# Optimization experiments

Measured on AMD Instinct MI355X. Metric: run time of the kernel, lower is better.

## Reference

```python
import jax, jax.numpy as jnp
import numpy as np

N = 50000
E = 800000
D = 128          # in_channels == hidden_channels
L = 3            # num_layers
JK = D * L       # jk 'cat' output
H2 = D // 2      # classifier hidden
C = 2            # out classes
EPS = 1e-5


def setup_inputs() -> dict:
    key = jax.random.key(0)
    ks = jax.random.split(key, 16)
    x = jax.random.normal(ks[0], (N, D), dtype=jnp.float32)
    edge_index = jax.random.randint(ks[1], (2, E), 0, N, dtype=jnp.int64)
    s = 0.05
    Wl = jax.random.normal(ks[2], (L, D, D), dtype=jnp.float32) * s   # lin_l (on aggregated), has bias
    bl = jax.random.normal(ks[3], (L, D), dtype=jnp.float32) * s
    Wr = jax.random.normal(ks[4], (L, D, D), dtype=jnp.float32) * s   # lin_r (on root), no bias
    gamma = jnp.ones((L, D), dtype=jnp.float32)
    beta = jnp.zeros((L, D), dtype=jnp.float32)
    rmean = jax.random.normal(ks[5], (L, D), dtype=jnp.float32) * s
    rvar = jax.random.uniform(ks[6], (L, D), dtype=jnp.float32, minval=0.5, maxval=1.5)
    Wc1 = jax.random.normal(ks[7], (JK, H2), dtype=jnp.float32) * s
    bc1 = jax.random.normal(ks[8], (H2,), dtype=jnp.float32) * s
    Wc2 = jax.random.normal(ks[9], (H2, C), dtype=jnp.float32) * s
    bc2 = jax.random.normal(ks[10], (C,), dtype=jnp.float32) * s
    return {"x": x, "edge_index": edge_index, "Wl": Wl, "bl": bl, "Wr": Wr,
            "gamma": gamma, "beta": beta, "rmean": rmean, "rvar": rvar,
            "Wc1": Wc1, "bc1": bc1, "Wc2": Wc2, "bc2": bc2}


def reference(x, edge_index, Wl, bl, Wr, gamma, beta, rmean, rvar, Wc1, bc1, Wc2, bc2):
    src, dst = edge_index[0], edge_index[1]
    # node in-degree (for mean aggregation), clamp to avoid div-by-zero
    deg = jax.ops.segment_sum(jnp.ones((E,), dtype=x.dtype), dst, num_segments=N)
    inv_deg = 1.0 / jnp.maximum(deg, 1.0)  # [N]

    h = x
    layer_outputs = []
    for i in range(L):
        # SAGEConv(mean): out = lin_l(mean_{j in N(i)} h_j) + lin_r(h_i)
        agg = jax.ops.segment_sum(h[src], dst, num_segments=N) * inv_deg[:, None]  # [N, D]
        h = agg @ Wl[i] + bl[i] + h @ Wr[i]
        # BatchNorm (eval: running stats), then ReLU; Dropout is identity in eval
        h = (h - rmean[i]) * jax.lax.rsqrt(rvar[i] + EPS) * gamma[i] + beta[i]
        h = jax.nn.relu(h)
        layer_outputs.append(h)

    jk = jnp.concatenate(layer_outputs, axis=-1)  # [N, L*D]
    z = jax.nn.relu(jk @ Wc1 + bc1)
    logits = z @ Wc2 + bc2  # [N, 2]
    return logits
```

## Files before the change

### kernel.cpp

```cpp
#include <hip/hip_runtime.h>
#include <hip/hip_fp16.h>
#include <cstdint>
#include <cstddef>

#define DD 128
#define JKD 384
#define EPSV 1e-5f
#define BSH 7
#define NBMAX 512
#define BCAP2 4096
#define PCH 8192
#define PTH 1024
#define BCAP 8192

typedef __attribute__((ext_vector_type(8))) short bf16x8;
typedef __attribute__((ext_vector_type(4))) float f32x4;
#define MFMA(a, b, c) __builtin_amdgcn_mfma_f32_16x16x32_bf16(a, b, c, 0, 0, 0)

__device__ inline unsigned short f2bf_rne(float f) {
  unsigned u = __float_as_uint(f);
  unsigned r = u + 0x7fffu + ((u >> 16) & 1u);
  return (unsigned short)(r >> 16);
}

__device__ inline void split8(const float* s, bf16x8& hi, bf16x8& lo) {
#pragma unroll
  for (int j = 0; j < 8; ++j) {
    float f = s[j];
    unsigned short h = f2bf_rne(f);
    float fh = __uint_as_float((unsigned)h << 16);
    hi[j] = (short)h;
    lo[j] = (short)f2bf_rne(f - fh);
  }
}

__device__ inline void h8_to_f8(uint4 raw, float* out) {
  const __half2* hp = reinterpret_cast<const __half2*>(&raw);
#pragma unroll
  for (int j = 0; j < 4; ++j) {
    float2 f = __half22float2(hp[j]);
    out[2 * j] = f.x;
    out[2 * j + 1] = f.y;
  }
}

__global__ void init_cursor(int* __restrict__ cursor) {
  int t = threadIdx.x;
  if (t < NBMAX) cursor[t] = t * BCAP2;
}

__global__ __launch_bounds__(PTH) void partition_prep(
    const int* __restrict__ src, const int* __restrict__ dst, int* bucket_cursor,
    unsigned* __restrict__ packed, int E, int nChunks,
    const float* __restrict__ Wl, const float* __restrict__ Wr, bf16x8* __restrict__ wf,
    const float* __restrict__ Wc1, bf16x8* __restrict__ wcf,
    const float* __restrict__ x, unsigned short* __restrict__ x16, int N) {
  __shared__ int h[NBMAX];
  __shared__ int lofs[NBMAX];
  __shared__ int res[NBMAX];
  __shared__ int lcur[NBMAX];
  __shared__ int wsum[4];
  __shared__ int wpref[4];
  __shared__ unsigned stage[PCH];

  if (blockIdx.x < nChunks) {
    int t = threadIdx.x;
    int lane = t & 63;
    int base = blockIdx.x * PCH;
    for (int i = t; i < NBMAX; i += PTH) h[i] = 0;
    __syncthreads();
#pragma unroll
    for (int it = 0; it < PCH / PTH; ++it) {
      int e = base + it * PTH + t;
      if (e < E) {
        int d = __builtin_nontemporal_load(dst + e);
        atomicAdd(&h[d >> BSH], 1);
      }
    }
    __syncthreads();
    int c0 = 0, c1 = 0, s = 0, sc = 0;
    if (t < 256) {
      c0 = h[2 * t];
      c1 = h[2 * t + 1];
      s = c0 + c1;
      sc = s;
#pragma unroll
      for (int off = 1; off < 64; off <<= 1) {
        int u = __shfl_up(sc, off, 64);
        if (lane >= off) sc += u;
      }
      if (lane == 63) wsum[t >> 6] = sc;
    }
    __syncthreads();
    if (t == 0) {
      int a = 0;
#pragma unroll
      for (int w = 0; w < 4; ++w) { wpref[w] = a; a += wsum[w]; }
    }
    __syncthreads();
    if (t < 256) {
      int excl = wpref[t >> 6] + sc - s;
      lofs[2 * t] = excl;
      lofs[2 * t + 1] = excl + c0;
      lcur[2 * t] = excl;
      lcur[2 * t + 1] = excl + c0;
      if (c0 > 0) res[2 * t] = atomicAdd(&bucket_cursor[2 * t], c0);
      if (c1 > 0) res[2 * t + 1] = atomicAdd(&bucket_cursor[2 * t + 1], c1);
    }
    __syncthreads();
#pragma unroll
    for (int it = 0; it < PCH / PTH; ++it) {
      int e = base + it * PTH + t;
      if (e < E) {
        int d = __builtin_nontemporal_load(dst + e);
        int sv = __builtin_nontemporal_load(src + e);
        int pos = atomicAdd(&lcur[d >> BSH], 1);
        stage[pos] = ((unsigned)(d & ((1 << BSH) - 1)) << 16) | (unsigned)(sv & 0xffff);
      }
    }
    __syncthreads();
    int wid = t >> 6;
    for (int b = wid; b < NBMAX; b += PTH / 64) {
      int run = h[b];
      if (run == 0) continue;
      int gbase = res[b], lbase = lofs[b];
      for (int j = lane; j < run; j += 64) packed[gbase + j] = stage[lbase + j];
    }
  } else {
    int sub = threadIdx.x >> 8;
    int t = threadIdx.x & 255;
    int f16blocks = (N * 16 + 255) / 256;
    int vb = (blockIdx.x - nChunks) * 4 + sub;
    if (vb >= 60 + f16blocks) return;
    if (vb < 48) {
      int idx = vb * 256 + t;
      int ln = idx & 63;
      int ksnt = (idx >> 6) & 31;
      int mat = (idx >> 11) & 1;
      int layer = idx >> 12;
      int ks = ksnt >> 3, nt = ksnt & 7;
      int nn = nt * 16 + (ln & 15);
      int k0 = ks * 32 + (ln >> 4) * 8;
      const float* W = (mat ? Wr : Wl) + (size_t)layer * DD * DD;
      float v[8];
#pragma unroll
      for (int j = 0; j < 8; ++j) v[j] = W[(size_t)(k0 + j) * DD + nn];
      bf16x8 hi, lo;
      split8(v, hi, lo);
      size_t base = (size_t)((layer * 2 + mat) * 2) * 2048 + (size_t)ksnt * 64 + ln;
      wf[base] = hi;
      wf[base + 2048] = lo;
    } else if (vb < 60) {
      int idx = (vb - 48) * 256 + t;
      int ln = idx & 63;
      int ksnt = idx >> 6;
      int ks = ksnt >> 2, nt = ksnt & 3;
      int nn = nt * 16 + (ln & 15);
      int k0 = ks * 32 + (ln >> 4) * 8;
      float v[8];
#pragma unroll
      for (int j = 0; j < 8; ++j) v[j] = Wc1[(size_t)(k0 + j) * 64 + nn];
      bf16x8 hi, lo;
      split8(v, hi, lo);
      wcf[idx] = hi;
      wcf[idx + 3072] = lo;
    } else {
      int idx = (vb - 60) * 256 + t;
      int r = idx >> 4, cc = (idx & 15) * 8;
      if (r < N) {
        const float* p = x + (size_t)r * DD + cc;
        float4 a = *reinterpret_cast<const float4*>(p);
        float4 bb = *reinterpret_cast<const float4*>(p + 4);
        __half2 h0 = __floats2half2_rn(a.x, a.y);
        __half2 h1 = __floats2half2_rn(a.z, a.w);
        __half2 h2 = __floats2half2_rn(bb.x, bb.y);
        __half2 h3 = __floats2half2_rn(bb.z, bb.w);
        uint4 o;
        o.x = *reinterpret_cast<unsigned*>(&h0);
        o.y = *reinterpret_cast<unsigned*>(&h1);
        o.z = *reinterpret_cast<unsigned*>(&h2);
        o.w = *reinterpret_cast<unsigned*>(&h3);
        *reinterpret_cast<uint4*>(x16 + (size_t)r * DD + cc) = o;
      }
    }
  }
}

__global__ __launch_bounds__(256) void csr_build(const unsigned* __restrict__ packed,
                                                 const int* __restrict__ bucket_cursor,
                                                 int* __restrict__ row_start,
                                                 int* __restrict__ row_end,
                                                 float* __restrict__ inv_deg,
                                                 unsigned short* __restrict__ col, int N) {
  __shared__ int cntA[128];
  __shared__ int lcur[128];
  __shared__ int wsum2[2];
  __shared__ int wpref2[2];
  __shared__ unsigned short stage[BCAP];
  int t = threadIdx.x;
  int b = blockIdx.x;
  int s0 = b * BCAP2;
  int cnt = bucket_cursor[b] - s0;
  if (t < 128) cntA[t] = 0;
  __syncthreads();
  for (int i = t; i < cnt; i += 256) {
    unsigned p = packed[s0 + i];
    atomicAdd(&cntA[p >> 16], 1);
  }
  __syncthreads();
  if (t < 128) {
    int lane = t & 63, wid = t >> 6;
    int v = cntA[t];
    int sc = v;
#pragma unroll
    for (int off = 1; off < 64; off <<= 1) {
      int u = __shfl_up(sc, off, 64);
      if (lane >= off) sc += u;
    }
    if (lane == 63) wsum2[wid] = sc;
    __syncthreads();
    if (t == 0) { wpref2[0] = 0; wpref2[1] = wsum2[0]; }
    __syncthreads();
    int excl = wpref2[wid] + sc - v;
    lcur[t] = excl;
    int node = b * 128 + t;
    if (node < N) {
      row_start[node] = s0 + excl;
      row_end[node] = s0 + excl + v;
      inv_deg[node] = 1.0f / fmaxf((float)v, 1.0f);
    }
  } else {
    __syncthreads();
    __syncthreads();
  }
  __syncthreads();
  for (int i = t; i < cnt; i += 256) {
    unsigned p = packed[s0 + i];
    int pos = atomicAdd(&lcur[p >> 16], 1);
    unsigned short us = (unsigned short)(p & 0xffff);
    if (pos < BCAP) stage[pos] = us;
    else col[s0 + pos] = us;
  }
  __syncthreads();
  int lim = min(cnt, BCAP);
  for (int i = t; i < lim; i += 256) col[s0 + i] = stage[i];
}

__global__ __launch_bounds__(256) void agg16_kernel(const unsigned short* __restrict__ h16,
                                                    int ldh,
                                                    const int* __restrict__ row_start,
                                                    const int* __restrict__ row_end,
                                                    const unsigned short* __restrict__ col,
                                                    const float* __restrict__ inv_deg,
                                                    unsigned short* __restrict__ agg16, int n) {
  int wib = threadIdx.x >> 6;
  int lane = threadIdx.x & 63;
  int node = blockIdx.x * 4 + wib;
  if (node >= n) return;
  int beg = row_start[node];
  int end = row_end[node];
  int q = lane >> 4, l15 = lane & 15;
  float acc[8];
#pragma unroll
  for (int k = 0; k < 8; ++k) acc[k] = 0.f;

  for (int j0 = beg; j0 < end; j0 += 16) {
    int cnt = end - j0;
    if (cnt > 16) cnt = 16;
    int cidx = (int)col[j0 + min(l15, cnt - 1)];
    uint4 raw[4];
    bool val[4];
#pragma unroll
    for (int k = 0; k < 4; ++k) {
      int e = k * 4 + q;
      int s = __shfl(cidx, e < cnt ? e : 0);
      val[k] = e < cnt;
      if (val[k]) raw[k] = *reinterpret_cast<const uint4*>(h16 + (size_t)s * ldh + l15 * 8);
    }
#pragma unroll
    for (int k = 0; k < 4; ++k) {
      if (val[k]) {
        float f8[8];
        h8_to_f8(raw[k], f8);
#pragma unroll
        for (int c = 0; c < 8; ++c) acc[c] += f8[c];
      }
    }
  }
#pragma unroll
  for (int m = 16; m <= 32; m <<= 1) {
#pragma unroll
    for (int k = 0; k < 8; ++k) acc[k] += __shfl_xor(acc[k], m);
  }
  if (lane < 16) {
    float w = inv_deg[node];
    __half2 h0 = __floats2half2_rn(acc[0] * w, acc[1] * w);
    __half2 h1 = __floats2half2_rn(acc[2] * w, acc[3] * w);
    __half2 h2 = __floats2half2_rn(acc[4] * w, acc[5] * w);
    __half2 h3 = __floats2half2_rn(acc[6] * w, acc[7] * w);
    uint4 o;
    o.x = *reinterpret_cast<unsigned*>(&h0);
    o.y = *reinterpret_cast<unsigned*>(&h1);
    o.z = *reinterpret_cast<unsigned*>(&h2);
    o.w = *reinterpret_cast<unsigned*>(&h3);
    *reinterpret_cast<uint4*>(agg16 + (size_t)node * DD + l15 * 8) = o;
  }
}

__global__ __launch_bounds__(256) void layer_gemm_mfma(
    const unsigned short* __restrict__ hin16, int ldh,
    const unsigned short* __restrict__ agg16,
    const bf16x8* __restrict__ Blh_g, const bf16x8* __restrict__ Bll_g,
    const bf16x8* __restrict__ Brh_g, const bf16x8* __restrict__ Brl_g,
    const float* __restrict__ bl, const float* __restrict__ gamma,
    const float* __restrict__ beta, const float* __restrict__ rmean,
    const float* __restrict__ rvar, unsigned short* __restrict__ out16, int n) {
  int t = threadIdx.x;
  int w = t >> 6, lane = t & 63;
  int lane16 = lane & 15, quad = lane >> 4;
  int row0 = blockIdx.x * 64;
  int m = row0 + w * 16 + lane16;
  bool valid = m < n;
  size_t mrow = (size_t)(valid ? m : 0);
  const unsigned short* ap = agg16 + mrow * DD + quad * 8;
  const unsigned short* hp = hin16 + mrow * (size_t)ldh + quad * 8;

  bf16x8 Ah[4], Al[4], Hh[4], Hl[4];
#pragma unroll
  for (int ks = 0; ks < 4; ++ks) {
    float a8[8], h8[8];
    if (valid) {
      uint4 ra = *reinterpret_cast<const uint4*>(ap + ks * 32);
      uint4 rh = *reinterpret_cast<const uint4*>(hp + ks * 32);
      h8_to_f8(ra, a8);
      h8_to_f8(rh, h8);
    } else {
#pragma unroll
      for (int j = 0; j < 8; ++j) { a8[j] = 0.f; h8[j] = 0.f; }
    }
    split8(a8, Ah[ks], Al[ks]);
    split8(h8, Hh[ks], Hl[ks]);
  }

  f32x4 acc[8];
#pragma unroll
  for (int nt = 0; nt < 8; ++nt) acc[nt] = (f32x4){0.f, 0.f, 0.f, 0.f};

#pragma unroll
  for (int ks = 0; ks < 4; ++ks) {
    int fb = ks * 8 * 64 + lane;
    bf16x8 B0[8], B1[8];
#pragma unroll
    for (int nt = 0; nt < 8; ++nt) B0[nt] = Blh_g[fb + nt * 64];
#pragma unroll
    for (int nt = 0; nt < 8; ++nt) acc[nt] = MFMA(Ah[ks], B0[nt], acc[nt]);
#pragma unroll
    for (int nt = 0; nt < 8; ++nt) B1[nt] = Bll_g[fb + nt * 64];
#pragma unroll
    for (int nt = 0; nt < 8; ++nt) acc[nt] = MFMA(Al[ks], B0[nt], acc[nt]);
#pragma unroll
    for (int nt = 0; nt < 8; ++nt) acc[nt] = MFMA(Ah[ks], B1[nt], acc[nt]);
#pragma unroll
    for (int nt = 0; nt < 8; ++nt) B0[nt] = Brh_g[fb + nt * 64];
#pragma unroll
    for (int nt = 0; nt < 8; ++nt) acc[nt] = MFMA(Hh[ks], B0[nt], acc[nt]);
#pragma unroll
    for (int nt = 0; nt < 8; ++nt) B1[nt] = Brl_g[fb + nt * 64];
#pragma unroll
    for (int nt = 0; nt < 8; ++nt) acc[nt] = MFMA(Hl[ks], B0[nt], acc[nt]);
#pragma unroll
    for (int nt = 0; nt < 8; ++nt) acc[nt] = MFMA(Hh[ks], B1[nt], acc[nt]);
  }

#pragma unroll
  for (int nt = 0; nt < 8; ++nt) {
    int c = nt * 16 + lane16;
    float sc = gamma[c] * rsqrtf(rvar[c] + EPSV);
    float sh = (bl[c] - rmean[c]) * sc + beta[c];
#pragma unroll
    for (int r = 0; r < 4; ++r) {
      int orow = row0 + w * 16 + quad * 4 + r;
      if (orow < n) {
        float v = fmaxf(fmaf(acc[nt][r], sc, sh), 0.f);
        __half hv = __float2half_rn(v);
        out16[(size_t)orow * JKD + c] = *reinterpret_cast<unsigned short*>(&hv);
      }
    }
  }
}

__global__ __launch_bounds__(256) void gemm2_cls(
    const unsigned short* __restrict__ gsrc, int ldg,
    const unsigned short* __restrict__ agg16,
    const bf16x8* __restrict__ Blh_g, const bf16x8* __restrict__ Bll_g,
    const bf16x8* __restrict__ Brh_g, const bf16x8* __restrict__ Brl_g,
    const float* __restrict__ bl, const float* __restrict__ gamma,
    const float* __restrict__ beta, const float* __restrict__ rmean,
    const float* __restrict__ rvar,
    const unsigned short* __restrict__ jk16, const bf16x8* __restrict__ wcf,
    const float* __restrict__ bc1, const float* __restrict__ Wc2,
    const float* __restrict__ bc2, float* __restrict__ out, int n) {
  __shared__ __align__(16) unsigned char smem[4 * 16 * 136 * 2];
  unsigned short (*sOut)[16][136] = reinterpret_cast<unsigned short(*)[16][136]>(smem);
  float (*sZ)[65] = reinterpret_cast<float(*)[65]>(smem);
  int t = threadIdx.x;
  int w = t >> 6, lane = t & 63;
  int lane16 = lane & 15, quad = lane >> 4;
  int row0 = blockIdx.x * 64;
  int m = row0 + w * 16 + lane16;
  bool valid = m < n;
  size_t mrow = (size_t)(valid ? m : 0);
  const unsigned short* ap = agg16 + mrow * DD + quad * 8;
  const unsigned short* hp = gsrc + mrow * (size_t)ldg + quad * 8;

  bf16x8 Ah[4], Al[4], Hh[4], Hl[4];
#pragma unroll
  for (int ks = 0; ks < 4; ++ks) {
    float a8[8], h8[8];
    if (valid) {
      uint4 ra = *reinterpret_cast<const uint4*>(ap + ks * 32);
      uint4 rh = *reinterpret_cast<const uint4*>(hp + ks * 32);
      h8_to_f8(ra, a8);
      h8_to_f8(rh, h8);
    } else {
#pragma unroll
      for (int j = 0; j < 8; ++j) { a8[j] = 0.f; h8[j] = 0.f; }
    }
    split8(a8, Ah[ks], Al[ks]);
    split8(h8, Hh[ks], Hl[ks]);
  }

  f32x4 acc[8];
#pragma unroll
  for (int nt = 0; nt < 8; ++nt) acc[nt] = (f32x4){0.f, 0.f, 0.f, 0.f};

#pragma unroll
  for (int ks = 0; ks < 4; ++ks) {
    int fb = ks * 8 * 64 + lane;
    bf16x8 B0[8], B1[8];
#pragma unroll
    for (int nt = 0; nt < 8; ++nt) B0[nt] = Blh_g[fb + nt * 64];
#pragma unroll
    for (int nt = 0; nt < 8; ++nt) acc[nt] = MFMA(Ah[ks], B0[nt], acc[nt]);
#pragma unroll
    for (int nt = 0; nt < 8; ++nt) B1[nt] = Bll_g[fb + nt * 64];
#pragma unroll
    for (int nt = 0; nt < 8; ++nt) acc[nt] = MFMA(Al[ks], B0[nt], acc[nt]);
#pragma unroll
    for (int nt = 0; nt < 8; ++nt) acc[nt] = MFMA(Ah[ks], B1[nt], acc[nt]);
#pragma unroll
    for (int nt = 0; nt < 8; ++nt) B0[nt] = Brh_g[fb + nt * 64];
#pragma unroll
    for (int nt = 0; nt < 8; ++nt) acc[nt] = MFMA(Hh[ks], B0[nt], acc[nt]);
#pragma unroll
    for (int nt = 0; nt < 8; ++nt) B1[nt] = Brl_g[fb + nt * 64];
#pragma unroll
    for (int nt = 0; nt < 8; ++nt) acc[nt] = MFMA(Hl[ks], B0[nt], acc[nt]);
#pragma unroll
    for (int nt = 0; nt < 8; ++nt) acc[nt] = MFMA(Hh[ks], B1[nt], acc[nt]);
  }

#pragma unroll
  for (int nt = 0; nt < 8; ++nt) {
    int c = nt * 16 + lane16;
    float sc = gamma[c] * rsqrtf(rvar[c] + EPSV);
    float sh = (bl[c] - rmean[c]) * sc + beta[c];
#pragma unroll
    for (int r = 0; r < 4; ++r) {
      float v = fmaxf(fmaf(acc[nt][r], sc, sh), 0.f);
      __half hv = __float2half_rn(v);
      sOut[w][quad * 4 + r][c] = *reinterpret_cast<unsigned short*>(&hv);
    }
  }
  __syncthreads();

  const unsigned short* jp = jk16 + mrow * JKD + quad * 8;
  f32x4 cacc[4];
#pragma unroll
  for (int nt = 0; nt < 4; ++nt) cacc[nt] = (f32x4){0.f, 0.f, 0.f, 0.f};

#pragma unroll
  for (int ks = 0; ks < 12; ++ks) {
    float a8[8];
    if (ks < 8) {
      if (valid) {
        uint4 raw = *reinterpret_cast<const uint4*>(jp + ks * 32);
        h8_to_f8(raw, a8);
      } else {
#pragma unroll
        for (int j = 0; j < 8; ++j) a8[j] = 0.f;
      }
    } else {
      uint4 raw = *reinterpret_cast<const uint4*>(&sOut[w][lane16][(ks - 8) * 32 + quad * 8]);
      h8_to_f8(raw, a8);
    }
    bf16x8 Jh, Jl;
    split8(a8, Jh, Jl);
    int fb = ks * 4 * 64 + lane;
    bf16x8 B0[4], B1[4];
#pragma unroll
    for (int nt = 0; nt < 4; ++nt) B0[nt] = wcf[fb + nt * 64];
#pragma unroll
    for (int nt = 0; nt < 4; ++nt) cacc[nt] = MFMA(Jh, B0[nt], cacc[nt]);
#pragma unroll
    for (int nt = 0; nt < 4; ++nt) B1[nt] = wcf[3072 + fb + nt * 64];
#pragma unroll
    for (int nt = 0; nt < 4; ++nt) cacc[nt] = MFMA(Jl, B0[nt], cacc[nt]);
#pragma unroll
    for (int nt = 0; nt < 4; ++nt) cacc[nt] = MFMA(Jh, B1[nt], cacc[nt]);
  }
  __syncthreads();

#pragma unroll
  for (int nt = 0; nt < 4; ++nt) {
    int c = nt * 16 + lane16;
    float b1 = bc1[c];
#pragma unroll
    for (int r = 0; r < 4; ++r)
      sZ[w * 16 + quad * 4 + r][c] = fmaxf(cacc[nt][r] + b1, 0.f);
  }
  __syncthreads();

  if (t < 128) {
    int r = t >> 1, j = t & 1;
    int gr = row0 + r;
    if (gr < n) {
      float s = bc2[j];
#pragma unroll
      for (int c = 0; c < 64; ++c) s = fmaf(sZ[r][c], Wc2[c * 2 + j], s);
      out[(size_t)gr * 2 + j] = s;
    }
  }
}


extern "C" void kernel_launch(void* const* d_in, const int* in_sizes, int n_in,
                              void* d_out, int out_size, void* d_ws, size_t ws_size,
                              hipStream_t stream) {
  const float* x = (const float*)d_in[0];
  const int* ei = (const int*)d_in[1];
  const float* Wl = (const float*)d_in[2];
  const float* bl = (const float*)d_in[3];
  const float* Wr = (const float*)d_in[4];
  const float* gamma = (const float*)d_in[5];
  const float* beta = (const float*)d_in[6];
  const float* rmean = (const float*)d_in[7];
  const float* rvar = (const float*)d_in[8];
  const float* Wc1 = (const float*)d_in[9];
  const float* bc1 = (const float*)d_in[10];
  const float* Wc2 = (const float*)d_in[11];
  const float* bc2 = (const float*)d_in[12];
  float* out = (float*)d_out;

  const int N = in_sizes[0] / DD;
  const int E = in_sizes[1] / 2;
  const int* src = ei;
  const int* dst = ei + E;

  auto align = [](size_t v) { return (v + 255) & ~(size_t)255; };
  char* ws = (char*)d_ws;
  size_t off = 0;
  int* row_start = (int*)(ws + off);  off = align(off + sizeof(int) * (size_t)N);
  int* row_end = (int*)(ws + off);    off = align(off + sizeof(int) * (size_t)N);
  unsigned short* col = (unsigned short*)(ws + off); off = align(off + sizeof(short) * (size_t)NBMAX * BCAP2);
  float* inv_deg = (float*)(ws + off); off = align(off + sizeof(float) * (size_t)N);
  unsigned* packed = (unsigned*)(ws + off); off = align(off + sizeof(unsigned) * (size_t)NBMAX * BCAP2);
  int* bucket_cursor = (int*)(ws + off); off = align(off + sizeof(int) * NBMAX);
  unsigned short* x16 = (unsigned short*)(ws + off);   off = align(off + sizeof(short) * (size_t)N * DD);
  unsigned short* agg16 = (unsigned short*)(ws + off); off = align(off + sizeof(short) * (size_t)N * DD);
  unsigned short* jk16 = (unsigned short*)(ws + off);  off = align(off + sizeof(short) * (size_t)N * JKD);
  bf16x8* wf = (bf16x8*)(ws + off);  off = align(off + (size_t)16 * 3 * 2 * 2 * 2048);
  bf16x8* wcf = (bf16x8*)(ws + off); off = align(off + (size_t)16 * 2 * 3072);

  const int nbuck = (N + 127) >> BSH;
  const int nChunks = (E + PCH - 1) / PCH;
  int f16blocks = (N * 16 + 255) / 256;
  int prepBlocks = (60 + f16blocks + 3) / 4;

  init_cursor<<<1, NBMAX, 0, stream>>>(bucket_cursor);
  partition_prep<<<nChunks + prepBlocks, PTH, 0, stream>>>(
      src, dst, bucket_cursor, packed, E, nChunks, Wl, Wr, wf, Wc1, wcf, x, x16, N);
  csr_build<<<nbuck, 256, 0, stream>>>(packed, bucket_cursor, row_start, row_end, inv_deg, col, N);

  int nTiles = (N + 63) / 64;
  for (int i = 0; i < 3; ++i) {
    const unsigned short* gsrc = (i == 0) ? x16 : (jk16 + (size_t)(i - 1) * DD);
    int ldg = (i == 0) ? DD : JKD;
    agg16_kernel<<<(N + 3) / 4, 256, 0, stream>>>(gsrc, ldg, row_start, row_end, col, inv_deg, agg16, N);
    bf16x8* Wlf = wf + (size_t)(i * 2 + 0) * 2 * 2048;
    bf16x8* Wrf = wf + (size_t)(i * 2 + 1) * 2 * 2048;
    if (i < 2) {
      layer_gemm_mfma<<<nTiles, 256, 0, stream>>>(
          gsrc, ldg, agg16, Wlf, Wlf + 2048, Wrf, Wrf + 2048,
          bl + (size_t)i * DD, gamma + (size_t)i * DD, beta + (size_t)i * DD,
          rmean + (size_t)i * DD, rvar + (size_t)i * DD, jk16 + (size_t)i * DD, N);
    } else {
      gemm2_cls<<<nTiles, 256, 0, stream>>>(
          gsrc, ldg, agg16, Wlf, Wlf + 2048, Wrf, Wrf + 2048,
          bl + (size_t)i * DD, gamma + (size_t)i * DD, beta + (size_t)i * DD,
          rmean + (size_t)i * DD, rvar + (size_t)i * DD,
          jk16, wcf, bc1, Wc2, bc2, out, N);
    }
  }
}
```

Measured before the change: 307.3 us.

## Stage GEMM weight fragments in LDS via global_load_lds

Both the layer GEMM and the fused last-layer/classifier kernel now cooperatively copy the pre-swizzled bf16 weight fragments into shared memory with async global-to-LDS loads, one K-slice at a time. The MFMA loops then read B operands from LDS instead of having every wave fetch them from global memory. The intent is to cut redundant global/L2 weight traffic, which is repeated per wave. In exchange it adds extra barriers per K-step, serialises load and compute, and raises LDS usage per block, which can lower occupancy.

```diff
diff --git a/kernel.cpp b/kernel.cpp
--- a/kernel.cpp
+++ b/kernel.cpp
@@ -42,6 +42,12 @@
     out[2 * j] = f.x;
     out[2 * j + 1] = f.y;
   }
+}
+
+__device__ __forceinline__ void gload16(const void* g, void* l) {
+  __builtin_amdgcn_global_load_lds(
+      (const __attribute__((address_space(1))) unsigned int*)g,
+      (__attribute__((address_space(3))) unsigned int*)l, 16, 0, 0);
 }
 
 __global__ void init_cursor(int* __restrict__ cursor) {
@@ -315,6 +321,7 @@
     const float* __restrict__ bl, const float* __restrict__ gamma,
     const float* __restrict__ beta, const float* __restrict__ rmean,
     const float* __restrict__ rvar, unsigned short* __restrict__ out16, int n) {
+  __shared__ __align__(16) unsigned char smem[32768];
   int t = threadIdx.x;
   int w = t >> 6, lane = t & 63;
   int lane16 = lane & 15, quad = lane >> 4;
@@ -325,6 +332,12 @@
   const unsigned short* ap = agg16 + mrow * DD + quad * 8;
   const unsigned short* hp = hin16 + mrow * (size_t)ldh + quad * 8;
 
+  const bf16x8* halfp = (w == 0) ? Blh_g : (w == 1) ? Bll_g : (w == 2) ? Brh_g : Brl_g;
+  unsigned char* sreg = smem + w * 8192;
+
+#pragma unroll
+  for (int c = 0; c < 8; ++c) gload16(halfp + c * 64 + lane, sreg + c * 1024);
+
   bf16x8 Ah[4], Al[4], Hh[4], Hl[4];
 #pragma unroll
   for (int ks = 0; ks < 4; ++ks) {
@@ -346,30 +359,39 @@
 #pragma unroll
   for (int nt = 0; nt < 8; ++nt) acc[nt] = (f32x4){0.f, 0.f, 0.f, 0.f};
 
+  const bf16x8* sB = reinterpret_cast<const bf16x8*>(smem);
+  __syncthreads();
+
 #pragma unroll
   for (int ks = 0; ks < 4; ++ks) {
-    int fb = ks * 8 * 64 + lane;
     bf16x8 B0[8], B1[8];
 #pragma unroll
-    for (int nt = 0; nt < 8; ++nt) B0[nt] = Blh_g[fb + nt * 64];
+    for (int nt = 0; nt < 8; ++nt) B0[nt] = sB[nt * 64 + lane];
 #pragma unroll
     for (int nt = 0; nt < 8; ++nt) acc[nt] = MFMA(Ah[ks], B0[nt], acc[nt]);
 #pragma unroll
-    for (int nt = 0; nt < 8; ++nt) B1[nt] = Bll_g[fb + nt * 64];
+    for (int nt = 0; nt < 8; ++nt) B1[nt] = sB[512 + nt * 64 + lane];
 #pragma unroll
     for (int nt = 0; nt < 8; ++nt) acc[nt] = MFMA(Al[ks], B0[nt], acc[nt]);
 #pragma unroll
     for (int nt = 0; nt < 8; ++nt) acc[nt] = MFMA(Ah[ks], B1[nt], acc[nt]);
 #pragma unroll
-    for (int nt = 0; nt < 8; ++nt) B0[nt] = Brh_g[fb + nt * 64];
+    for (int nt = 0; nt < 8; ++nt) B0[nt] = sB[1024 + nt * 64 + lane];
 #pragma unroll
     for (int nt = 0; nt < 8; ++nt) acc[nt] = MFMA(Hh[ks], B0[nt], acc[nt]);
 #pragma unroll
-    for (int nt = 0; nt < 8; ++nt) B1[nt] = Brl_g[fb + nt * 64];
+    for (int nt = 0; nt < 8; ++nt) B1[nt] = sB[1536 + nt * 64 + lane];
 #pragma unroll
     for (int nt = 0; nt < 8; ++nt) acc[nt] = MFMA(Hl[ks], B0[nt], acc[nt]);
 #pragma unroll
     for (int nt = 0; nt < 8; ++nt) acc[nt] = MFMA(Hh[ks], B1[nt], acc[nt]);
+    if (ks < 3) {
+      __syncthreads();
+#pragma unroll
+      for (int c = 0; c < 8; ++c)
+        gload16(halfp + (ks + 1) * 512 + c * 64 + lane, sreg + c * 1024);
+      __syncthreads();
+    }
   }
 
 #pragma unroll
@@ -400,9 +422,12 @@
     const unsigned short* __restrict__ jk16, const bf16x8* __restrict__ wcf,
     const float* __restrict__ bc1, const float* __restrict__ Wc2,
     const float* __restrict__ bc2, float* __restrict__ out, int n) {
-  __shared__ __align__(16) unsigned char smem[4 * 16 * 136 * 2];
+  __shared__ __align__(16) unsigned char smem[17408 + 24576];
   unsigned short (*sOut)[16][136] = reinterpret_cast<unsigned short(*)[16][136]>(smem);
   float (*sZ)[65] = reinterpret_cast<float(*)[65]>(smem);
+  unsigned char* clsw = smem + 17408;
+  const bf16x8* sB = reinterpret_cast<const bf16x8*>(smem);
+  const bf16x8* csB = reinterpret_cast<const bf16x8*>(clsw);
   int t = threadIdx.x;
   int w = t >> 6, lane = t & 63;
   int lane16 = lane & 15, quad = lane >> 4;
@@ -413,6 +438,12 @@
   const unsigned short* ap = agg16 + mrow * DD + quad * 8;
   const unsigned short* hp = gsrc + mrow * (size_t)ldg + quad * 8;
 
+  const bf16x8* halfp = (w == 0) ? Blh_g : (w == 1) ? Bll_g : (w == 2) ? Brh_g : Brl_g;
+  unsigned char* sreg = smem + w * 8192;
+
+#pragma unroll
+  for (int c = 0; c < 8; ++c) gload16(halfp + c * 64 + lane, sreg + c * 1024);
+
   bf16x8 Ah[4], Al[4], Hh[4], Hl[4];
 #pragma unroll
   for (int ks = 0; ks < 4; ++ks) {
@@ -434,31 +465,40 @@
 #pragma unroll
   for (int nt = 0; nt < 8; ++nt) acc[nt] = (f32x4){0.f, 0.f, 0.f, 0.f};
 
+  __syncthreads();
+
 #pragma unroll
   for (int ks = 0; ks < 4; ++ks) {
-    int fb = ks * 8 * 64 + lane;
     bf16x8 B0[8], B1[8];
 #pragma unroll
-    for (int nt = 0; nt < 8; ++nt) B0[nt] = Blh_g[fb + nt * 64];
+    for (int nt = 0; nt < 8; ++nt) B0[nt] = sB[nt * 64 + lane];
 #pragma unroll
     for (int nt = 0; nt < 8; ++nt) acc[nt] = MFMA(Ah[ks], B0[nt], acc[nt]);
 #pragma unroll
-    for (int nt = 0; nt < 8; ++nt) B1[nt] = Bll_g[fb + nt * 64];
+    for (int nt = 0; nt < 8; ++nt) B1[nt] = sB[512 + nt * 64 + lane];
 #pragma unroll
     for (int nt = 0; nt < 8; ++nt) acc[nt] = MFMA(Al[ks], B0[nt], acc[nt]);
 #pragma unroll
     for (int nt = 0; nt < 8; ++nt) acc[nt] = MFMA(Ah[ks], B1[nt], acc[nt]);
 #pragma unroll
-    for (int nt = 0; nt < 8; ++nt) B0[nt] = Brh_g[fb + nt * 64];
+    for (int nt = 0; nt < 8; ++nt) B0[nt] = sB[1024 + nt * 64 + lane];
 #pragma unroll
     for (int nt = 0; nt < 8; ++nt) acc[nt] = MFMA(Hh[ks], B0[nt], acc[nt]);
 #pragma unroll
-    for (int nt = 0; nt < 8; ++nt) B1[nt] = Brl_g[fb + nt * 64];
+    for (int nt = 0; nt < 8; ++nt) B1[nt] = sB[1536 + nt * 64 + lane];
 #pragma unroll
     for (int nt = 0; nt < 8; ++nt) acc[nt] = MFMA(Hl[ks], B0[nt], acc[nt]);
 #pragma unroll
     for (int nt = 0; nt < 8; ++nt) acc[nt] = MFMA(Hh[ks], B1[nt], acc[nt]);
-  }
+    if (ks < 3) {
+      __syncthreads();
+#pragma unroll
+      for (int c = 0; c < 8; ++c)
+        gload16(halfp + (ks + 1) * 512 + c * 64 + lane, sreg + c * 1024);
+      __syncthreads();
+    }
+  }
+  __syncthreads();
 
 #pragma unroll
   for (int nt = 0; nt < 8; ++nt) {
@@ -472,7 +512,6 @@
       sOut[w][quad * 4 + r][c] = *reinterpret_cast<unsigned short*>(&hv);
     }
   }
-  __syncthreads();
 
   const unsigned short* jp = jk16 + mrow * JKD + quad * 8;
   f32x4 cacc[4];
@@ -480,34 +519,46 @@
   for (int nt = 0; nt < 4; ++nt) cacc[nt] = (f32x4){0.f, 0.f, 0.f, 0.f};
 
 #pragma unroll
-  for (int ks = 0; ks < 12; ++ks) {
-    float a8[8];
-    if (ks < 8) {
-      if (valid) {
-        uint4 raw = *reinterpret_cast<const uint4*>(jp + ks * 32);
+  for (int g = 0; g < 4; ++g) {
+    __syncthreads();
+#pragma unroll
+    for (int c = 0; c < 6; ++c) {
+      int ch = w * 6 + c;
+      const bf16x8* gp = (ch < 12) ? (wcf + g * 768 + ch * 64)
+                                   : (wcf + 3072 + g * 768 + (ch - 12) * 64);
+      gload16(gp + lane, clsw + ch * 1024);
+    }
+    __syncthreads();
+#pragma unroll
+    for (int k3 = 0; k3 < 3; ++k3) {
+      int ks = g * 3 + k3;
+      float a8[8];
+      if (ks < 8) {
+        if (valid) {
+          uint4 raw = *reinterpret_cast<const uint4*>(jp + ks * 32);
+          h8_to_f8(raw, a8);
+        } else {
+#pragma unroll
+          for (int j = 0; j < 8; ++j) a8[j] = 0.f;
+        }
+      } else {
+        uint4 raw = *reinterpret_cast<const uint4*>(&sOut[w][lane16][(ks - 8) * 32 + quad * 8]);
         h8_to_f8(raw, a8);
-      } else {
-#pragma unroll
-        for (int j = 0; j < 8; ++j) a8[j] = 0.f;
       }
-    } else {
-      uint4 raw = *reinterpret_cast<const uint4*>(&sOut[w][lane16][(ks - 8) * 32 + quad * 8]);
-      h8_to_f8(raw, a8);
-    }
-    bf16x8 Jh, Jl;
-    split8(a8, Jh, Jl);
-    int fb = ks * 4 * 64 + lane;
-    bf16x8 B0[4], B1[4];
-#pragma unroll
-    for (int nt = 0; nt < 4; ++nt) B0[nt] = wcf[fb + nt * 64];
-#pragma unroll
-    for (int nt = 0; nt < 4; ++nt) cacc[nt] = MFMA(Jh, B0[nt], cacc[nt]);
-#pragma unroll
-    for (int nt = 0; nt < 4; ++nt) B1[nt] = wcf[3072 + fb + nt * 64];
-#pragma unroll
-    for (int nt = 0; nt < 4; ++nt) cacc[nt] = MFMA(Jl, B0[nt], cacc[nt]);
-#pragma unroll
-    for (int nt = 0; nt < 4; ++nt) cacc[nt] = MFMA(Jh, B1[nt], cacc[nt]);
+      bf16x8 Jh, Jl;
+      split8(a8, Jh, Jl);
+      bf16x8 B0[4], B1[4];
+#pragma unroll
+      for (int nt = 0; nt < 4; ++nt) B0[nt] = csB[k3 * 256 + nt * 64 + lane];
+#pragma unroll
+      for (int nt = 0; nt < 4; ++nt) cacc[nt] = MFMA(Jh, B0[nt], cacc[nt]);
+#pragma unroll
+      for (int nt = 0; nt < 4; ++nt) B1[nt] = csB[768 + k3 * 256 + nt * 64 + lane];
+#pragma unroll
+      for (int nt = 0; nt < 4; ++nt) cacc[nt] = MFMA(Jl, B0[nt], cacc[nt]);
+#pragma unroll
+      for (int nt = 0; nt < 4; ++nt) cacc[nt] = MFMA(Jh, B1[nt], cacc[nt]);
+    }
   }
   __syncthreads();
 
```

After: 284.3 us. 1.08x faster.
